# Kernel optimization log

Measured on AMD Instinct MI355X. Metric: run time of the kernel, lower is better.

## Reference

```python
import jax, jax.numpy as jnp
import numpy as np

B, R, N, DN, DR, H, Q, NB = 32, 10, 512, 128, 128, 128, 256, 16


def setup_inputs() -> dict:
    key = jax.random.key(0)
    ks = jax.random.split(key, 14)
    inp = {
        'node_features': jax.random.normal(ks[0], (B, N, DN), jnp.float32),
        'relation_features': jax.random.normal(ks[1], (B, R, DR), jnp.float32),
        'adj': jax.random.uniform(ks[2], (B, R, N, N), jnp.float32),
        'obs': jax.random.normal(ks[3], (B, Q, H), jnp.float32),
        'node_mask': jnp.ones((B, N), jnp.float32),
        'obs_mask': jnp.ones((B, Q), jnp.float32),
        # RGCN params (single layer: hidden_dims=[128])
        'Wb': jax.random.normal(ks[4], (NB, (DN + DR) * R), jnp.float32) * 0.02,  # bottleneck (no bias)
        'Ww': jax.random.normal(ks[5], (H, NB), jnp.float32) * 0.1,               # weight (no bias)
        'rgcn_bias': jnp.zeros((), jnp.float32),                                   # scalar bias (filled 0)
        # ContextQueryAttention params
        'w_C': jax.random.normal(ks[6], (H,), jnp.float32) * 0.05,
        'w_Q': jax.random.normal(ks[7], (H,), jnp.float32) * 0.05,
        'w_CQ': jax.random.normal(ks[8], (H,), jnp.float32) * 0.05,
        'cq_bias': jnp.zeros((), jnp.float32),
        # ReprAggregator output linear (shared for both directions)
        'lin_W': jax.random.normal(ks[9], (H, 4 * H), jnp.float32) * 0.02,
        'lin_b': jnp.zeros((H,), jnp.float32),
    }
    return inp


def _masked_softmax(s, mask, axis):
    return jax.nn.softmax(jnp.where(mask > 0, s, -jnp.inf), axis=axis)


def _rgcn(node_features, relation_features, adj, Wb, Ww, rgcn_bias):
    b, n = node_features.shape[0], node_features.shape[1]
    # per-relation concat: (B,R,N,DN+DR)
    nf = jnp.broadcast_to(node_features[:, None], (b, R, n, node_features.shape[-1]))
    rf = jnp.broadcast_to(relation_features[:, :, None, :], (b, R, n, relation_features.shape[-1]))
    cat = jnp.concatenate([nf, rf], axis=-1)
    # per-relation bmm, gathered in relation order along feature dim: (B,N,R*(DN+DR))
    sup = jnp.einsum('brnm,brmd->bnrd', adj, cat)
    sup = sup.reshape(b, n, R * cat.shape[-1])
    h = sup @ Wb.T            # (B,N,NB)
    h = h @ Ww.T              # (B,N,H)
    return jax.nn.sigmoid(h + rgcn_bias)


def _cqattn(ctx, query, ctx_mask, query_mask, w_C, w_Q, w_CQ, cq_bias):
    # trilinear similarity: (B,Lc,Lq)
    res_C = ctx @ w_C                                  # (B,Lc)
    res_Q = query @ w_Q                                # (B,Lq)
    res_CQ = jnp.einsum('bch,bqh->bcq', ctx * w_CQ, query)
    S = res_C[:, :, None] + res_Q[:, None, :] + res_CQ + cq_bias
    s_ctx = _masked_softmax(S, ctx_mask[:, :, None], axis=1)     # softmax over ctx dim
    s_query = _masked_softmax(S, query_mask[:, None, :], axis=2)  # softmax over query dim
    P = jnp.einsum('bcq,bqh->bch', s_query, query)
    Qm = jnp.einsum('bcq,bdq,bdh->bch', s_query, s_ctx, ctx)
    return jnp.concatenate([ctx, P, ctx * P, ctx * Qm], axis=-1)  # (B,Lc,4H)


def reference(node_features, relation_features, adj, obs, node_mask, obs_mask,
              Wb, Ww, rgcn_bias, w_C, w_Q, w_CQ, cq_bias, lin_W, lin_b):
    # GraphEncoder (single RGCN layer)
    node_repr = _rgcn(node_features, relation_features, adj, Wb, Ww, rgcn_bias)
    # ReprAggregator between obs text repr and node repr
    a1 = _cqattn(obs, node_repr, obs_mask, node_mask, w_C, w_Q, w_CQ, cq_bias)
    a2 = _cqattn(node_repr, obs, node_mask, obs_mask, w_C, w_Q, w_CQ, cq_bias)
    h_og = a1 @ lin_W.T + lin_b   # (B,Q,H)
    h_go = a2 @ lin_W.T + lin_b   # (B,N,H)
    return h_og, h_go
```

## Files before the change

kernel.cpp:

```cpp
#include <hip/hip_runtime.h>
#include <hip/hip_bf16.h>
#include <stdint.h>

typedef unsigned short u16;
typedef __attribute__((ext_vector_type(8))) short short8;
typedef __attribute__((ext_vector_type(4))) float f32x4;

#define DEVI static __device__ __forceinline__

constexpr int B = 32, R = 10, N = 512, H = 128, Q = 256, NB = 16;
constexpr int KWB = 2560;

DEVI u16 f2u(float f) { return __builtin_bit_cast(unsigned short, __float2bfloat16(f)); }
DEVI float u2f(u16 u) { union { uint32_t i; float f; } c; c.i = ((uint32_t)u) << 16; return c.f; }

DEVI float wredmax(float v) { for (int o = 32; o; o >>= 1) v = fmaxf(v, __shfl_xor(v, o)); return v; }
DEVI float wredsum(float v) { for (int o = 32; o; o >>= 1) v += __shfl_xor(v, o); return v; }

DEVI short8 cvt8(const float* p) {
  float4 f0 = *(const float4*)p;
  float4 f1 = *(const float4*)(p + 4);
  short8 v;
  v[0] = (short)f2u(f0.x); v[1] = (short)f2u(f0.y);
  v[2] = (short)f2u(f0.z); v[3] = (short)f2u(f0.w);
  v[4] = (short)f2u(f1.x); v[5] = (short)f2u(f1.y);
  v[6] = (short)f2u(f1.z); v[7] = (short)f2u(f1.w);
  return v;
}

__global__ __launch_bounds__(256) void k_prep(
    const float* __restrict__ linW, u16* __restrict__ linWb,
    const float* __restrict__ Wb, u16* __restrict__ WbB,
    const float* __restrict__ Ww, u16* __restrict__ WwB,
    const float* __restrict__ rf, float* __restrict__ vv,
    const float* __restrict__ obs, const float* __restrict__ wC,
    const float* __restrict__ wQ, const float* __restrict__ wCQ,
    u16* __restrict__ obsW, float* __restrict__ a_o, float* __restrict__ d_o,
    u16* __restrict__ obsT) {
  int bid = blockIdx.x, t = threadIdx.x;
  __shared__ float sa[4], sd[4];
  __shared__ u16 tile[32][33];
  if (bid < 64) {
    int i = bid * 256 + t;
    float4 f = ((const float4*)linW)[i];
    ushort4 o;
    o.x = f2u(f.x); o.y = f2u(f.y); o.z = f2u(f.z); o.w = f2u(f.w);
    ((ushort4*)linWb)[i] = o;
  } else if (bid < 144) {
    int rk = (bid - 64) * 2 + (t >> 7);
    int d = t & 127;
    int r = rk / NB, k = rk % NB;
    WbB[(long)rk * 128 + d] = f2u(Wb[(long)k * KWB + r * 256 + d]);
  } else if (bid < 160) {
    int idx = (bid - 144) * 256 + t;
    int h = idx >> 5, kb = idx & 31;
    WwB[idx] = (kb < NB) ? f2u(Ww[h * NB + kb]) : (u16)0;
  } else if (bid < 1440) {
    int w = t >> 6, lane = t & 63;
    int gid = (bid - 160) * 4 + w;
    int b = gid / (R * NB), rk = gid % (R * NB), r = rk / NB, k = rk % NB;
    float s = 0.f;
    for (int dd = 0; dd < 2; ++dd) {
      int d = lane + dd * 64;
      s += rf[((long)b * R + r) * H + d] * Wb[(long)k * KWB + r * 256 + 128 + d];
    }
    s = wredsum(s);
    if (lane == 0) vv[((long)b * R + r) * NB + k] = s;
  } else if (bid < 5536) {
    int row = (bid - 1440) * 2 + (t >> 7);
    int tt = t & 127;
    float x = obs[(long)row * H + tt];
    obsW[(long)row * H + tt] = f2u(x * wCQ[tt]);
    float aa = wredsum(x * wC[tt]);
    float dd2 = wredsum(x * wQ[tt]);
    int wv = t >> 6;
    if ((t & 63) == 0) { sa[wv] = aa; sd[wv] = dd2; }
    __syncthreads();
    if ((t & 127) == 0) {
      int h = t >> 7;
      a_o[row] = sa[h * 2] + sa[h * 2 + 1];
      d_o[row] = sd[h * 2] + sd[h * 2 + 1];
    }
  } else {
    int id = bid - 5536;
    int cx = id & 3, ry = (id >> 2) & 7, b = id >> 5;
    int c0 = cx * 32, r0 = ry * 32;
    int tx = t & 31, ty = t >> 5;
    for (int i = 0; i < 4; i++) {
      int r = r0 + ty + i * 8, c = c0 + tx;
      tile[ty + i * 8][tx] = f2u(obs[((long)b * Q + r) * H + c]);
    }
    __syncthreads();
    for (int i = 0; i < 4; i++) {
      int c = c0 + ty + i * 8, r = r0 + tx;
      obsT[((long)b * H + c) * Q + r] = tile[tx][ty + i * 8];
    }
  }
}

__global__ __launch_bounds__(512) void k_tt(const u16* __restrict__ WbB, const float* __restrict__ nf,
                                            const float* __restrict__ vv, u16* __restrict__ tT) {
  int f = blockIdx.x + 4 * blockIdx.y;
  int g = (f & 7) * 16 + (f >> 3);
  int bx = g & 3, b = g >> 2;
  int t = threadIdx.x;
  __shared__ __align__(16) u16 tile[128][128];
  {
    int row = t >> 2, q = (t & 3) * 32;
    const float* src = nf + ((long)b * N + bx * 128 + row) * H + q;
    int sw = (row & 7) << 3;
    for (int j = 0; j < 4; j++) {
      short8 v = cvt8(src + j * 8);
      *(short8*)&tile[row][(q + j * 8) ^ sw] = v;
    }
  }
  __syncthreads();
  int w = t >> 6, lane = t & 63;
  int rw = lane & 15, kq = lane >> 4;
  for (int r = w; r < R; r += 8) {
    f32x4 acc[8] = {};
    for (int kit = 0; kit < H; kit += 32) {
      short8 av = *(const short8*)(WbB + ((long)r * NB + rw) * 128 + kit + kq * 8);
#pragma unroll
      for (int nt = 0; nt < 8; nt++) {
        int brow = nt * 16 + rw;
        short8 bv = *(const short8*)&tile[brow][(kit + kq * 8) ^ ((brow & 7) << 3)];
        acc[nt] = __builtin_amdgcn_mfma_f32_16x16x32_bf16(av, bv, acc[nt], 0, 0, 0);
      }
    }
    long rbase = (long)(b * R + r) * NB;
#pragma unroll
    for (int nt = 0; nt < 8; nt++) {
      int gc = bx * 128 + nt * 16 + rw;
      for (int i = 0; i < 4; i++) {
        int gr = kq * 4 + i;
        tT[(rbase + gr) * N + gc] = f2u(acc[nt][i] + vv[rbase + gr]);
      }
    }
  }
}

__global__ __launch_bounds__(512) void k_rgcn(
    const float* __restrict__ adj, const u16* __restrict__ tT,
    const u16* __restrict__ WwB, const float* __restrict__ rb,
    const float* __restrict__ wC, const float* __restrict__ wQ,
    u16* __restrict__ nr, u16* __restrict__ nrT,
    float* __restrict__ b_n, float* __restrict__ c_n) {
  int f = blockIdx.x + 32 * blockIdx.y;
  int g = (f & 7) * 128 + (f >> 3);
  int ntile = g & 31, b = g >> 5;
  int n0 = ntile * 16;
  int tid = threadIdx.x;
  int w = tid >> 6, lane = tid & 63;
  int rw = lane & 15, kq = lane >> 4;
  __shared__ float hred[8][16][17];
  __shared__ __align__(16) u16 hbf[16][32];
  __shared__ float bpc[8][16][2];
  float rbv = rb[0];

  f32x4 acc = {0.f, 0.f, 0.f, 0.f};
#pragma unroll 4
  for (int j = 0; j < 20; ++j) {
    int kkk = w + 8 * j;
    int r = kkk >> 4, k = (kkk & 15) * 32;
    short8 av = cvt8(adj + (((long)(b * R + r) * N) + n0 + rw) * N + k + kq * 8);
    short8 bv = *(const short8*)(tT + ((long)(b * R + r) * NB + rw) * N + k + kq * 8);
    acc = __builtin_amdgcn_mfma_f32_16x16x32_bf16(av, bv, acc, 0, 0, 0);
  }
  for (int i = 0; i < 4; i++) hred[w][kq * 4 + i][rw] = acc[i];
  __syncthreads();
  if (tid < 256) {
    int n = tid >> 4, kb = tid & 15;
    float s = 0.f;
    for (int ww = 0; ww < 8; ww++) s += hred[ww][n][kb];
    hbf[n][kb] = f2u(s);
    hbf[n][kb + 16] = 0;
  }
  __syncthreads();

  short8 av = *(const short8*)&hbf[rw][kq * 8];
  short8 bv = *(const short8*)(WwB + (long)(w * 16 + rw) * 32 + kq * 8);
  f32x4 a2 = {0.f, 0.f, 0.f, 0.f};
  a2 = __builtin_amdgcn_mfma_f32_16x16x32_bf16(av, bv, a2, 0, 0, 0);
  int h = w * 16 + rw;
  float wq = wQ[h], wc = wC[h];
  float bsum[4], csum[4];
  for (int i = 0; i < 4; i++) {
    float s = 1.f / (1.f + expf(-(a2[i] + rbv)));
    int n = n0 + kq * 4 + i;
    u16 sv = f2u(s);
    nr[((long)b * N + n) * H + h] = sv;
    nrT[((long)b * H + h) * N + n] = sv;
    bsum[i] = s * wq;
    csum[i] = s * wc;
  }
  for (int i = 0; i < 4; i++) {
    for (int o = 8; o; o >>= 1) { bsum[i] += __shfl_xor(bsum[i], o); csum[i] += __shfl_xor(csum[i], o); }
  }
  if (rw == 0)
    for (int i = 0; i < 4; i++) { bpc[w][kq * 4 + i][0] = bsum[i]; bpc[w][kq * 4 + i][1] = csum[i]; }
  __syncthreads();
  if (tid < 32) {
    int ns = tid & 15, which = tid >> 4;
    float s = 0.f;
    for (int ww = 0; ww < 8; ww++) s += bpc[ww][ns][which];
    (which ? c_n : b_n)[(long)b * N + n0 + ns] = s;
  }
}

__global__ __launch_bounds__(512) void k_mm_soft(
    const u16* __restrict__ obsW, const u16* __restrict__ nr,
    const float* __restrict__ b_n, const float* __restrict__ c_n,
    const float* __restrict__ nmask,
    u16* __restrict__ sq1, u16* __restrict__ sc2, u16* __restrict__ ST) {
  int f = blockIdx.x + 16 * blockIdx.y;
  int g = (f & 7) * 64 + (f >> 3);
  int mt = g & 15, b = g >> 4;
  int tid = threadIdx.x;
  int w = tid >> 6, lane = tid & 63;
  int rw = lane & 15, kq = lane >> 4;
  __shared__ float sm1[8][16], sm2[8][16], ss1[8][16], ss2[8][16];

  const u16* ap = obsW + ((long)b * Q + mt * 16 + rw) * H + kq * 8;
  const u16* bp = nr + ((long)b * N + w * 64 + rw) * H + kq * 8;
  f32x4 acc[4] = {};
  for (int k = 0; k < H; k += 32) {
    short8 av = *(const short8*)(ap + k);
#pragma unroll
    for (int nt = 0; nt < 4; nt++) {
      short8 bv = *(const short8*)(bp + (long)nt * 16 * H + k);
      acc[nt] = __builtin_amdgcn_mfma_f32_16x16x32_bf16(av, bv, acc[nt], 0, 0, 0);
    }
  }
  float bn[4], cn[4];
  bool mk[4];
  int gcv[4];
#pragma unroll
  for (int nt = 0; nt < 4; nt++) {
    int gc = w * 64 + nt * 16 + rw;
    gcv[nt] = gc;
    mk[nt] = nmask[(long)b * N + gc] > 0.f;
    bn[nt] = b_n[(long)b * N + gc];
    cn[nt] = c_n[(long)b * N + gc];
  }
#pragma unroll
  for (int nt = 0; nt < 4; nt++) {
    long stb = ((long)b * N + gcv[nt]) * Q + mt * 16 + kq * 4;
    for (int i = 0; i < 4; i++) ST[stb + i] = f2u(acc[nt][i]);
  }
  float m1[4], m2[4];
  for (int i = 0; i < 4; i++) { m1[i] = -1e30f; m2[i] = -1e30f; }
#pragma unroll
  for (int nt = 0; nt < 4; nt++)
    for (int i = 0; i < 4; i++) {
      float s = acc[nt][i];
      if (mk[nt]) { m1[i] = fmaxf(m1[i], s + bn[nt]); m2[i] = fmaxf(m2[i], s + cn[nt]); }
    }
  for (int i = 0; i < 4; i++)
    for (int o = 8; o; o >>= 1) { m1[i] = fmaxf(m1[i], __shfl_xor(m1[i], o)); m2[i] = fmaxf(m2[i], __shfl_xor(m2[i], o)); }
  if (rw == 0)
    for (int i = 0; i < 4; i++) { sm1[w][kq * 4 + i] = m1[i]; sm2[w][kq * 4 + i] = m2[i]; }
  __syncthreads();
  for (int i = 0; i < 4; i++) {
    float g1 = -1e30f, g2 = -1e30f;
    for (int ww = 0; ww < 8; ww++) { g1 = fmaxf(g1, sm1[ww][kq * 4 + i]); g2 = fmaxf(g2, sm2[ww][kq * 4 + i]); }
    m1[i] = g1; m2[i] = g2;
  }
  float e1[4][4], e2[4][4];
  float s1[4] = {0.f, 0.f, 0.f, 0.f}, s2[4] = {0.f, 0.f, 0.f, 0.f};
#pragma unroll
  for (int nt = 0; nt < 4; nt++)
    for (int i = 0; i < 4; i++) {
      float s = acc[nt][i];
      float a = mk[nt] ? expf(s + bn[nt] - m1[i]) : 0.f;
      float c = mk[nt] ? expf(s + cn[nt] - m2[i]) : 0.f;
      e1[nt][i] = a; e2[nt][i] = c;
      s1[i] += a; s2[i] += c;
    }
  for (int i = 0; i < 4; i++)
    for (int o = 8; o; o >>= 1) { s1[i] += __shfl_xor(s1[i], o); s2[i] += __shfl_xor(s2[i], o); }
  if (rw == 0)
    for (int i = 0; i < 4; i++) { ss1[w][kq * 4 + i] = s1[i]; ss2[w][kq * 4 + i] = s2[i]; }
  __syncthreads();
  float r1[4], r2[4];
  for (int i = 0; i < 4; i++) {
    float g1 = 0.f, g2 = 0.f;
    for (int ww = 0; ww < 8; ww++) { g1 += ss1[ww][kq * 4 + i]; g2 += ss2[ww][kq * 4 + i]; }
    r1[i] = 1.f / g1; r2[i] = 1.f / g2;
  }
#pragma unroll
  for (int nt = 0; nt < 4; nt++)
    for (int i = 0; i < 4; i++) {
      long ob = ((long)b * Q + mt * 16 + kq * 4 + i) * N + gcv[nt];
      sq1[ob] = f2u(e1[nt][i] * r1[i]);
      sc2[ob] = f2u(e2[nt][i] * r2[i]);
    }
}

__global__ __launch_bounds__(256) void k_soft_col(
    const u16* __restrict__ ST, const float* __restrict__ a_o, const float* __restrict__ d_o,
    const float* __restrict__ omask, u16* __restrict__ sc1T, u16* __restrict__ sq2) {
  int w = threadIdx.x >> 6, lane = threadIdx.x & 63;
  long rn = (long)blockIdx.x * 4 + w;
  int b = (int)(rn >> 9);
  float v1[4], v2[4];
  const u16* st = ST + rn * Q + lane * 4;
  for (int i = 0; i < 4; i++) {
    int o = lane * 4 + i;
    float mv = u2f(st[i]);
    bool on = omask[(long)b * Q + o] > 0.f;
    v1[i] = on ? a_o[(long)b * Q + o] + mv : -1e30f;
    v2[i] = on ? d_o[(long)b * Q + o] + mv : -1e30f;
  }
  float m1 = wredmax(fmaxf(fmaxf(v1[0], v1[1]), fmaxf(v1[2], v1[3])));
  float m2 = wredmax(fmaxf(fmaxf(v2[0], v2[1]), fmaxf(v2[2], v2[3])));
  float e1[4], e2[4], s1 = 0.f, s2 = 0.f;
  for (int i = 0; i < 4; i++) {
    e1[i] = expf(v1[i] - m1); e2[i] = expf(v2[i] - m2);
    s1 += e1[i]; s2 += e2[i];
  }
  s1 = wredsum(s1); s2 = wredsum(s2);
  float r1 = 1.f / s1, r2 = 1.f / s2;
  for (int i = 0; i < 4; i++) {
    sc1T[rn * Q + lane * 4 + i] = f2u(e1[i] * r1);
    sq2[rn * Q + lane * 4 + i] = f2u(e2[i] * r2);
  }
}

DEVI void gemm_tile(const u16* A, const u16* Bt, u16* C, int Mdim, int Kdim,
                    long sA, long sBt, long sC, int tc, int batch, int mt, int lane) {
  if (mt * 16 >= Mdim) return;
  int rw = lane & 15, kq = lane >> 4;
  const u16* ap = A + (long)batch * sA + (long)(mt * 16 + rw) * Kdim + kq * 8;
  const u16* bp = Bt + (long)batch * sBt + (long)rw * Kdim + kq * 8;
  f32x4 acc[8] = {};
  for (int k = 0; k < Kdim; k += 32) {
    short8 av = *(const short8*)(ap + k);
#pragma unroll
    for (int nt = 0; nt < 8; nt++) {
      short8 bv = *(const short8*)(bp + (long)nt * 16 * Kdim + k);
      acc[nt] = __builtin_amdgcn_mfma_f32_16x16x32_bf16(av, bv, acc[nt], 0, 0, 0);
    }
  }
#pragma unroll
  for (int nt = 0; nt < 8; nt++) {
    int gc = nt * 16 + rw;
    for (int i = 0; i < 4; i++) {
      int gr = mt * 16 + kq * 4 + i;
      long idx = tc ? ((long)gc * Mdim + gr) : ((long)gr * H + gc);
      C[(long)batch * sC + idx] = f2u(acc[nt][i]);
    }
  }
}

__global__ __launch_bounds__(64) void k_gemmA(
    const u16* __restrict__ sq1, const u16* __restrict__ sc2,
    const u16* __restrict__ sc1T, const u16* __restrict__ sq2,
    const u16* __restrict__ nrT, const u16* __restrict__ obsT,
    u16* __restrict__ P1, u16* __restrict__ T2T, u16* __restrict__ T1T, u16* __restrict__ P2) {
  int bid = blockIdx.x;
  int t = (bid & 7) * 512 + (bid >> 3);
  int z = t >> 10, rem = t & 1023, batch = rem >> 5, mt = rem & 31;
  int lane = threadIdx.x;
  if (z == 0)      gemm_tile(sq1,  nrT,  P1,  Q, N, (long)Q * N, (long)H * N, (long)Q * H, 0, batch, mt, lane);
  else if (z == 1) gemm_tile(sc2,  nrT,  T2T, Q, N, (long)Q * N, (long)H * N, (long)H * Q, 1, batch, mt, lane);
  else if (z == 2) gemm_tile(sc1T, obsT, T1T, N, Q, (long)N * Q, (long)H * Q, (long)H * N, 1, batch, mt, lane);
  else             gemm_tile(sq2,  obsT, P2,  N, Q, (long)N * Q, (long)H * Q, (long)N * H, 0, batch, mt, lane);
}

__global__ __launch_bounds__(64) void k_gemmB(
    const u16* __restrict__ sq1, const u16* __restrict__ sq2,
    const u16* __restrict__ T1T, const u16* __restrict__ T2T,
    u16* __restrict__ Qm1, u16* __restrict__ Qm2) {
  int bid = blockIdx.x;
  int t = (bid & 7) * 256 + (bid >> 3);
  int z = t >> 10, rem = t & 1023, batch = rem >> 5, mt = rem & 31;
  int lane = threadIdx.x;
  if (z == 0) gemm_tile(sq1, T1T, Qm1, Q, N, (long)Q * N, (long)H * N, (long)Q * H, 0, batch, mt, lane);
  else        gemm_tile(sq2, T2T, Qm2, N, Q, (long)N * Q, (long)H * Q, (long)N * H, 0, batch, mt, lane);
}

__global__ __launch_bounds__(64) void k_cat(
    const float* __restrict__ obs, const u16* __restrict__ nrr,
    const u16* __restrict__ P1, const u16* __restrict__ Qm1,
    const u16* __restrict__ P2, const u16* __restrict__ Qm2,
    const u16* __restrict__ Wt, const float* __restrict__ bias,
    float* __restrict__ out0, float* __restrict__ out1) {
  int bid = blockIdx.x;
  int t = (bid & 7) * 256 + (bid >> 3);
  int z = t >> 10, rem = t & 1023, batch = rem >> 5, mt = rem & 31;
  int Mdim = z ? N : Q;
  if (mt * 16 >= Mdim) return;
  const u16* P = z ? P2 : P1;
  const u16* Qm = z ? Qm2 : Qm1;
  float* out = z ? out1 : out0;
  int lane = threadIdx.x;
  int rw = lane & 15, kq = lane >> 4;
  long arow = (long)batch * Mdim + mt * 16 + rw;
  const u16* bp = Wt + (long)rw * (4 * H) + kq * 8;
  f32x4 acc[8] = {};
  for (int k = 0; k < 4 * H; k += 32) {
    int sec = k >> 7;
    int off = (k & 127) + kq * 8;
    long rb2 = arow * H + off;
    short8 av;
    if (sec == 0) {
      if (!z) av = cvt8(obs + rb2);
      else    av = *(const short8*)(nrr + rb2);
    } else if (sec == 1) {
      av = *(const short8*)(P + rb2);
    } else {
      float xf[8];
      if (!z) {
        const float* xp = obs + rb2;
        float4 f0 = *(const float4*)xp;
        float4 f1 = *(const float4*)(xp + 4);
        xf[0] = f0.x; xf[1] = f0.y; xf[2] = f0.z; xf[3] = f0.w;
        xf[4] = f1.x; xf[5] = f1.y; xf[6] = f1.z; xf[7] = f1.w;
      } else {
        short8 xv = *(const short8*)(nrr + rb2);
        for (int i = 0; i < 8; i++) xf[i] = u2f((u16)xv[i]);
      }
      short8 pv = *(const short8*)((sec == 2 ? P : Qm) + rb2);
      for (int i = 0; i < 8; i++) av[i] = (short)f2u(xf[i] * u2f((u16)pv[i]));
    }
#pragma unroll
    for (int nt = 0; nt < 8; nt++) {
      short8 bv = *(const short8*)(bp + (long)nt * 16 * (4 * H) + k);
      acc[nt] = __builtin_amdgcn_mfma_f32_16x16x32_bf16(av, bv, acc[nt], 0, 0, 0);
    }
  }
#pragma unroll
  for (int nt = 0; nt < 8; nt++) {
    int gc = nt * 16 + rw;
    float cb = bias[gc];
    for (int i = 0; i < 4; i++) {
      int gr = mt * 16 + kq * 4 + i;
      out[((long)batch * Mdim + gr) * H + gc] = acc[nt][i] + cb;
    }
  }
}

extern "C" void kernel_launch(void* const* d_in, const int* in_sizes, int n_in,
                              void* d_out, int out_size, void* d_ws, size_t ws_size,
                              hipStream_t stream) {
  const float* nf    = (const float*)d_in[0];
  const float* rf    = (const float*)d_in[1];
  const float* adj   = (const float*)d_in[2];
  const float* obs   = (const float*)d_in[3];
  const float* nmask = (const float*)d_in[4];
  const float* omask = (const float*)d_in[5];
  const float* Wb    = (const float*)d_in[6];
  const float* Ww    = (const float*)d_in[7];
  const float* rb    = (const float*)d_in[8];
  const float* wC    = (const float*)d_in[9];
  const float* wQ    = (const float*)d_in[10];
  const float* wCQ   = (const float*)d_in[11];
  const float* linW  = (const float*)d_in[13];
  const float* linb  = (const float*)d_in[14];
  float* outp = (float*)d_out;

  char* w = (char*)d_ws;
  auto alloc = [&](size_t bytes) { char* p = w; w += (bytes + 255) & ~(size_t)255; return p; };
  u16*   linWb = (u16*)  alloc((size_t)H * 4 * H * 2);
  u16*   WbB   = (u16*)  alloc((size_t)R * NB * 128 * 2);
  u16*   WwB   = (u16*)  alloc((size_t)H * 32 * 2);
  float* vv    = (float*)alloc((size_t)B * R * NB * 4);
  u16*   obsW  = (u16*)  alloc((size_t)B * Q * H * 2);
  u16*   obsT  = (u16*)  alloc((size_t)B * H * Q * 2);
  float* a_o   = (float*)alloc((size_t)B * Q * 4);
  float* d_o   = (float*)alloc((size_t)B * Q * 4);
  float* b_n   = (float*)alloc((size_t)B * N * 4);
  float* c_n   = (float*)alloc((size_t)B * N * 4);
  u16*   nr    = (u16*)  alloc((size_t)B * N * H * 2);
  u16*   nrT   = (u16*)  alloc((size_t)B * H * N * 2);
  u16*   tT    = (u16*)  alloc((size_t)B * R * NB * N * 2);
  u16*   ST    = (u16*)  alloc((size_t)B * N * Q * 2);
  u16*   sq1   = (u16*)  alloc((size_t)B * Q * N * 2);
  u16*   sc2   = (u16*)  alloc((size_t)B * Q * N * 2);
  u16*   sc1T  = (u16*)  alloc((size_t)B * N * Q * 2);
  u16*   sq2   = (u16*)  alloc((size_t)B * N * Q * 2);
  u16*   P1    = (u16*)  alloc((size_t)B * Q * H * 2);
  u16*   T1T   = (u16*)  alloc((size_t)B * H * N * 2);
  u16*   Qm1   = (u16*)  alloc((size_t)B * Q * H * 2);
  u16*   P2    = (u16*)  alloc((size_t)B * N * H * 2);
  u16*   T2T   = (u16*)  alloc((size_t)B * H * Q * 2);
  u16*   Qm2   = (u16*)  alloc((size_t)B * N * H * 2);
  float* out1  = outp + (long)B * Q * H;

  k_prep<<<6560, 256, 0, stream>>>(linW, linWb, Wb, WbB, Ww, WwB,
                                   rf, vv, obs, wC, wQ, wCQ, obsW, a_o, d_o, obsT);
  k_tt<<<dim3(N / 128, B), 512, 0, stream>>>(WbB, nf, vv, tT);
  k_rgcn<<<dim3(N / 16, B), 512, 0, stream>>>(adj, tT, WwB, rb, wC, wQ, nr, nrT, b_n, c_n);
  k_mm_soft<<<dim3(Q / 16, B), 512, 0, stream>>>(obsW, nr, b_n, c_n, nmask, sq1, sc2, ST);
  k_soft_col<<<B * N / 4, 256, 0, stream>>>(ST, a_o, d_o, omask, sc1T, sq2);
  k_gemmA<<<4096, 64, 0, stream>>>(sq1, sc2, sc1T, sq2, nrT, obsT, P1, T2T, T1T, P2);
  k_gemmB<<<2048, 64, 0, stream>>>(sq1, sq2, T1T, T2T, Qm1, Qm2);
  k_cat<<<2048, 64, 0, stream>>>(obs, nr, P1, Qm1, P2, Qm2, linWb, linb, outp, out1);

  (void)in_sizes; (void)n_in; (void)out_size; (void)ws_size;
}
```

Measured before the change: 284.8 us.

## Double-buffer adj tiles into LDS via async global_load_lds in RGCN kernel

The RGCN aggregation now streams each relation's 16x512 fp32 adj tile into a double-buffered, XOR-swizzled LDS buffer using global_load_lds. The next relation's load is issued while the current one is consumed by MFMA. This replaces the direct per-lane global loads, aiming to overlap the memory-bound adj read with compute and to coalesce it. The cost is 64KB of LDS per block, which can limit occupancy, plus a barrier per relation. Correctness depends on the async LDS loads completing before the barrier.

New measurement: 276.4 us. 2.9% less time.

```diff
diff --git a/kernel.cpp b/kernel.cpp
--- a/kernel.cpp
+++ b/kernel.cpp
@@ -26,6 +26,12 @@
   v[4] = (short)f2u(f1.x); v[5] = (short)f2u(f1.y);
   v[6] = (short)f2u(f1.z); v[7] = (short)f2u(f1.w);
   return v;
+}
+
+DEVI void gload16(const float* gp, void* lp) {
+  __builtin_amdgcn_global_load_lds(
+      (__attribute__((address_space(1))) void*)(uintptr_t)gp,
+      (__attribute__((address_space(3))) void*)lp, 16, 0, 0);
 }
 
 __global__ __launch_bounds__(256) void k_prep(
@@ -153,20 +159,51 @@
   int tid = threadIdx.x;
   int w = tid >> 6, lane = tid & 63;
   int rw = lane & 15, kq = lane >> 4;
+  __shared__ __align__(16) float abuf[2][16][512];
   __shared__ float hred[8][16][17];
   __shared__ __align__(16) u16 hbf[16][32];
   __shared__ float bpc[8][16][2];
   float rbv = rb[0];
 
+  auto stage = [&](int pb, int r) {
+    long rowstart = (long)(b * R + r) * N + n0;
+#pragma unroll
+    for (int ci = 0; ci < 4; ci++) {
+      int c = w + ci * 8;
+      int ro = c >> 1, h = c & 1;
+      int sg = h * 64 + lane;
+      int gg = sg ^ (ro & 7);
+      const float* gp = adj + (rowstart + ro) * N + gg * 4;
+      gload16(gp, (void*)&abuf[pb][ro][h * 256]);
+    }
+  };
+
   f32x4 acc = {0.f, 0.f, 0.f, 0.f};
-#pragma unroll 4
-  for (int j = 0; j < 20; ++j) {
-    int kkk = w + 8 * j;
-    int r = kkk >> 4, k = (kkk & 15) * 32;
-    short8 av = cvt8(adj + (((long)(b * R + r) * N) + n0 + rw) * N + k + kq * 8);
-    short8 bv = *(const short8*)(tT + ((long)(b * R + r) * NB + rw) * N + k + kq * 8);
-    acc = __builtin_amdgcn_mfma_f32_16x16x32_bf16(av, bv, acc, 0, 0, 0);
-  }
+  stage(0, 0);
+  __syncthreads();
+  for (int r = 0; r < R; r++) {
+    int pb = r & 1;
+    if (r + 1 < R) stage(pb ^ 1, r + 1);
+    const u16* tb = tT + ((long)(b * R + r) * NB + rw) * N;
+#pragma unroll
+    for (int i = 0; i < 2; i++) {
+      int kcol = w * 64 + i * 32 + kq * 8;
+      int gr0 = kcol >> 2;
+      int sg0 = gr0 ^ (rw & 7);
+      int sg1 = (gr0 + 1) ^ (rw & 7);
+      float4 a0 = *(const float4*)&abuf[pb][rw][sg0 * 4];
+      float4 a1 = *(const float4*)&abuf[pb][rw][sg1 * 4];
+      short8 av;
+      av[0] = (short)f2u(a0.x); av[1] = (short)f2u(a0.y);
+      av[2] = (short)f2u(a0.z); av[3] = (short)f2u(a0.w);
+      av[4] = (short)f2u(a1.x); av[5] = (short)f2u(a1.y);
+      av[6] = (short)f2u(a1.z); av[7] = (short)f2u(a1.w);
+      short8 bv = *(const short8*)(tb + kcol);
+      acc = __builtin_amdgcn_mfma_f32_16x16x32_bf16(av, bv, acc, 0, 0, 0);
+    }
+    __syncthreads();
+  }
+
   for (int i = 0; i < 4; i++) hred[w][kq * 4 + i][rw] = acc[i];
   __syncthreads();
   if (tid < 256) {
```
